# Kernel optimization log

Measured on AMD Instinct MI355X. Metric: run time of the kernel, lower is better.

Reference implementation:

```python
import jax, jax.numpy as jnp
import numpy as np
import math

# dims matching init_kwargs
B, N, CS, CZ = 1, 512, 384, 128
H, C, PQ, PV = 8, 128, 8, 8
INF, EPS = 1e5, 1e-8

# ---- quaternion / motor helpers (PGA motor encoded as [qw,qx,qy,qz,tx,ty,tz,0]) ----

def quat_conj(q):
    return q * jnp.array([1.0, -1.0, -1.0, -1.0], q.dtype)

def quat_mul(a, b):
    aw, ax, ay, az = jnp.split(a, 4, -1)
    bw, bx, by, bz = jnp.split(b, 4, -1)
    return jnp.concatenate([
        aw*bw - ax*bx - ay*by - az*bz,
        aw*bx + ax*bw + ay*bz - az*by,
        aw*by - ax*bz + ay*bw + az*bx,
        aw*bz + ax*by - ay*bx + az*bw], -1)

def quat_rotate(q, v):
    qv = q[..., 1:]
    uv = jnp.cross(qv, v)
    uuv = jnp.cross(qv, uv)
    return v + 2.0 * (q[..., :1] * uv + uuv)

def point_trafo(p, q, t):
    # p [...,K,3]; rigid transform by frame motor, homogeneous 4-vector out
    pp = quat_rotate(q, p) + t
    return jnp.concatenate([pp, jnp.ones_like(pp[..., :1])], -1)

def mv_transform(mv, q, t):
    # versor sandwich on a 16-dim multivector: three rotatable 3-vector blocks,
    # the point block (7:10, weight at 10) also translates; slots 0 and 10:16 invariant
    s0 = mv[..., 0:1]
    v1 = quat_rotate(q, mv[..., 1:4])
    v2 = quat_rotate(q, mv[..., 4:7])
    w = mv[..., 10:11]
    p = quat_rotate(q, mv[..., 7:10]) + w * t
    return jnp.concatenate([s0, v1, v2, p, mv[..., 10:16]], -1)

def mv_transform_inv(mv, q, t):
    qc = quat_conj(q)
    s0 = mv[..., 0:1]
    v1 = quat_rotate(qc, mv[..., 1:4])
    v2 = quat_rotate(qc, mv[..., 4:7])
    w = mv[..., 10:11]
    p = quat_rotate(qc, mv[..., 7:10] - w * t)
    return jnp.concatenate([s0, v1, v2, p, mv[..., 10:16]], -1)


def _forward(s, g, z, T, mask, W_q, b_q, W_kv, b_kv, W_qp, b_qp, W_kp, b_kp,
             W_vg, b_vg, W_mg, W_b, b_b, W_dz, b_dz, head_weights,
             softmax_weights, W_out, b_out, W_geo):
    T8 = T[..., :8]                                      # extract_motor
    qn = T8[..., :4]
    qn = qn / jnp.sqrt(jnp.sum(qn**2, -1, keepdims=True) + EPS)
    tr = T8[..., 4:7]

    q = (s @ W_q + b_q).reshape(B, N, H, C)
    kv = (s @ W_kv + b_kv).reshape(B, N, H, 2 * C)
    k, v = kv[..., :C], kv[..., C:]

    def make_pts(W, bb):
        # split into 3 chunks + stack(dim=-1) == reshape(...,3,HP).swapaxes
        p = (s @ W + bb).reshape(B, N, 3, H * PQ).swapaxes(-1, -2)  # [B,N,HP,3]
        p4 = point_trafo(p, qn[:, :, None, :], tr[:, :, None, :])
        return p4.reshape(B, N, H, PQ, 4)

    q_pts = make_pts(W_qp, b_qp)
    k_pts = make_pts(W_kp, b_kp)

    v_g = (s @ W_vg + b_vg).reshape(B, N, PV, 16)
    v_g = jnp.einsum('oi,bnic->bnoc', W_mg,
                     jnp.concatenate([v_g, g], -2)).reshape(B, N, H, PV, 16)

    bias = jnp.einsum('bijz,zh->bhij', z, W_b) + b_b[None, :, None, None]
    a = jnp.einsum('bihc,bjhc->bhij', q, k) * math.sqrt(1.0 / (3 * C))
    a = a + math.sqrt(1.0 / 3.0) * bias

    disp = q_pts[:, :, None, :, :, :3] - k_pts[:, None, :, :, :, :3]  # [B,N,N,H,P,3]
    pt = jnp.sum(disp**2, -1)                                         # [B,N,N,H,P]
    hw = jax.nn.softplus(head_weights) * math.sqrt(1.0 / (3 * (PQ * 9.0 / 2)))
    pt = -0.5 * jnp.sum(pt * hw[None, None, None, :, None], -1)       # [B,N,N,H]

    sq_mask = INF * (mask[:, :, None] * mask[:, None, :] - 1.0)
    a = a + pt.transpose(0, 3, 1, 2) + sq_mask[:, None]
    a = jax.nn.softmax(softmax_weights[None, :, None, None] * a, axis=-1)

    o = jnp.einsum('bhij,bjhc->bihc', a, v)                           # [B,N,H,C]

    qb, tb = qn[:, :, None, None, :], tr[:, :, None, None, :]
    vg_glob = mv_transform(v_g, qb, tb)
    o_g = jnp.einsum('bhij,bjhpc->bihpc', a, vg_glob)
    o_g = mv_transform_inv(o_g, qb, tb)                               # [B,N,H,PV,16]
    n1 = jnp.sqrt(jnp.sum(o_g[..., :10]**2, -1) + EPS)
    n2 = jnp.sqrt(jnp.sum(o_g[..., 10:]**2, -1) + EPS)
    o_g_norm = jnp.stack([n1, n2], -1)                                # [B,N,H,PV,2]

    # local relative frame features (8 per head)
    q_rel = quat_mul(quat_conj(qn)[:, :, None, :], qn[:, None, :, :])
    t_rel = quat_rotate(quat_conj(qn)[:, :, None, :], tr[:, None, :, :] - tr[:, :, None, :])
    rel = jnp.concatenate([q_rel, t_rel, jnp.zeros_like(t_rel[..., :1])], -1)  # [B,N,N,8]
    o_rel = jnp.einsum('bhij,bijc->bihc', a, rel)

    o_pair = jnp.einsum('bhij,bijc->bihc', a, z @ W_dz + b_dz)        # [B,N,H,CZ//4]

    feats = jnp.concatenate([o_pair, o, o_rel,
                             o_g.reshape(B, N, H, PV * 16),
                             o_g_norm.reshape(B, N, H, PV * 2)], -1).reshape(B, N, -1)
    s_out = feats @ W_out + b_out                                     # [B,N,CS]
    g_out = jnp.einsum('oi,bnic->bnoc', W_geo, o_g.reshape(B, N, H * PV, 16))
    return s_out, g_out


def setup_inputs() -> dict:
    key = jax.random.key(0)
    ks = jax.random.split(key, 32)
    def rn(i, shape, sc=1.0):
        return sc * jax.random.normal(ks[i], shape, jnp.float32)
    s = rn(0, (B, N, CS))
    g = rn(1, (B, N, PV, 16))
    z = rn(2, (B, N, N, CZ))
    Traw = rn(3, (B, N, 16))
    qn = Traw[..., :4]
    qn = qn / jnp.sqrt(jnp.sum(qn**2, -1, keepdims=True) + 1e-8)
    T = Traw.at[..., :4].set(qn).at[..., 4:7].multiply(3.0).at[..., 7:].set(0.0)
    mask = jnp.ones((B, N), jnp.float32)
    w = 0.02
    CAT = H * (CZ // 4 + C + 8 + PV * 18)   # 2496
    return dict(
        s=s, g=g, z=z, T=T, mask=mask,
        W_q=rn(4, (CS, H * C), w), b_q=jnp.zeros((H * C,), jnp.float32),
        W_kv=rn(5, (CS, 2 * H * C), w), b_kv=jnp.zeros((2 * H * C,), jnp.float32),
        W_qp=rn(6, (CS, H * PQ * 3), w), b_qp=jnp.zeros((H * PQ * 3,), jnp.float32),
        W_kp=rn(7, (CS, H * PQ * 3), w), b_kp=jnp.zeros((H * PQ * 3,), jnp.float32),
        W_vg=rn(8, (CS, PV * 16), w), b_vg=jnp.zeros((PV * 16,), jnp.float32),
        W_mg=rn(9, (H * PV, 2 * PV), 0.1),
        W_b=rn(10, (CZ, H), w), b_b=jnp.zeros((H,), jnp.float32),
        W_dz=rn(11, (CZ, CZ // 4), w), b_dz=jnp.zeros((CZ // 4,), jnp.float32),
        head_weights=-2.0 + 0.3 * rn(12, (H,)),
        softmax_weights=jnp.ones((H,), jnp.float32) + 0.1 * rn(13, (H,)),
        W_out=rn(14, (CAT, CS), w), b_out=jnp.zeros((CS,), jnp.float32),
        W_geo=rn(15, (PV, H * PV), 0.1))


def reference(s, g, z, T, mask, W_q, b_q, W_kv, b_kv, W_qp, b_qp, W_kp, b_kp,
              W_vg, b_vg, W_mg, W_b, b_b, W_dz, b_dz, head_weights,
              softmax_weights, W_out, b_out, W_geo):
    return _forward(s, g, z, T, mask, W_q, b_q, W_kv, b_kv, W_qp, b_qp, W_kp,
                    b_kp, W_vg, b_vg, W_mg, W_b, b_b, W_dz, b_dz, head_weights,
                    softmax_weights, W_out, b_out, W_geo)
```

## Files before the change

kernel.cpp:

```cpp
#include <hip/hip_runtime.h>
#include <math.h>

#define NN 512
#define CSD 384
#define CZD 128
#define HD 8
#define CD 128
#define EPSV 1e-8f
#define INFV 100000.0f

#define OFF_QN    ((size_t)0)
#define OFF_TR    ((size_t)2048)
#define OFF_ROWT  ((size_t)4096)
#define OFF_COLT  ((size_t)8192)
#define OFF_SB    ((size_t)12288)
#define OFF_QBUF  ((size_t)45056)
#define OFF_KV    ((size_t)569344)
#define OFF_QPR   ((size_t)1617920)
#define OFF_KPR   ((size_t)1716224)
#define OFF_VGR   ((size_t)1814528)
#define OFF_ZB    ((size_t)1880064)
#define OFF_A     ((size_t)3977216)
#define OFF_U     ((size_t)6074368)
#define OFF_V     ((size_t)6729728)
#define OFF_VP    ((size_t)7385088)
#define OFF_OB0   ((size_t)8433664)
#define OFF_OB1   ((size_t)8957952)
#define OFF_OG0   ((size_t)9482240)
#define OFF_OG1   ((size_t)10006528)
#define OFF_FEATS ((size_t)10530816)
#define OFF_PS    ((size_t)11808768)

typedef __attribute__((ext_vector_type(4))) float f32x4;
typedef __attribute__((ext_vector_type(8))) short bf16x8;
typedef __attribute__((ext_vector_type(4))) short s16x4;

__device__ __forceinline__ void qrot(const float q[4], const float* v, float* out) {
    float qw = q[0], qx = q[1], qy = q[2], qz = q[3];
    float ux = qy*v[2] - qz*v[1];
    float uy = qz*v[0] - qx*v[2];
    float uz = qx*v[1] - qy*v[0];
    float uux = qy*uz - qz*uy;
    float uuy = qz*ux - qx*uz;
    float uuz = qx*uy - qy*ux;
    out[0] = v[0] + 2.0f*(qw*ux + uux);
    out[1] = v[1] + 2.0f*(qw*uy + uuy);
    out[2] = v[2] + 2.0f*(qw*uz + uuz);
}

__device__ __forceinline__ void cvt2(float x, unsigned short& h, unsigned short& lo) {
    unsigned u = __float_as_uint(x);
    unsigned r = (u + 0x7FFFu + ((u >> 16) & 1u)) >> 16;
    h = (unsigned short)r;
    float hf = __uint_as_float(r << 16);
    float lf = x - hf;
    unsigned u2 = __float_as_uint(lf);
    unsigned r2 = (u2 + 0x7FFFu + ((u2 >> 16) & 1u)) >> 16;
    lo = (unsigned short)r2;
}

__device__ __forceinline__ void stA(short* H, short* L, int row, int k4, float4 v) {
    unsigned short h0,l0,h1,l1,h2,l2,h3,l3;
    cvt2(v.x,h0,l0); cvt2(v.y,h1,l1); cvt2(v.z,h2,l2); cvt2(v.w,h3,l3);
    s16x4 vh = {(short)h0,(short)h1,(short)h2,(short)h3};
    s16x4 vl = {(short)l0,(short)l1,(short)l2,(short)l3};
    *(s16x4*)(H + row*40 + k4) = vh;
    *(s16x4*)(L + row*40 + k4) = vl;
}
__device__ __forceinline__ void stBT(short* H, short* L, int k, int n4, float4 v) {
    unsigned short h, lo;
    cvt2(v.x,h,lo); H[(n4+0)*40+k]=(short)h; L[(n4+0)*40+k]=(short)lo;
    cvt2(v.y,h,lo); H[(n4+1)*40+k]=(short)h; L[(n4+1)*40+k]=(short)lo;
    cvt2(v.z,h,lo); H[(n4+2)*40+k]=(short)h; L[(n4+2)*40+k]=(short)lo;
    cvt2(v.w,h,lo); H[(n4+3)*40+k]=(short)h; L[(n4+3)*40+k]=(short)lo;
}

template<int BT>
__device__ __forceinline__ void mfma_tiles(const float* __restrict__ A, int lda,
                                           const float* __restrict__ B, int ldb,
                                           int m0, int n0, int k0, int nk,
                                           f32x4* acc,
                                           short* Ah, short* Al, short* Bh, short* Bl) {
    int t = threadIdx.x;
    int w = t >> 6, l = t & 63, g = l >> 4, li = l & 15;
    int ar = t >> 3, ak = (t & 7) << 2;
    const float* Ap0 = A + (size_t)(m0 + ar)*lda + ak;
    const float* Ap1 = A + (size_t)(m0 + ar + 32)*lda + ak;
    const float* Bp0; const float* Bp1;
    int bk = t >> 4, bn = (t & 15) << 2;
    if (BT) {
        Bp0 = B + (size_t)(n0 + ar)*ldb + ak;
        Bp1 = B + (size_t)(n0 + ar + 32)*ldb + ak;
    } else {
        Bp0 = B + (size_t)bk*ldb + n0 + bn;
        Bp1 = B + (size_t)(bk + 16)*ldb + n0 + bn;
    }
    float4 a0 = *(const float4*)(Ap0 + k0);
    float4 a1 = *(const float4*)(Ap1 + k0);
    float4 b0, b1;
    if (BT) { b0 = *(const float4*)(Bp0 + k0); b1 = *(const float4*)(Bp1 + k0); }
    else    { b0 = *(const float4*)(Bp0 + (size_t)k0*ldb); b1 = *(const float4*)(Bp1 + (size_t)k0*ldb); }
    for (int kc = 0; kc < nk; kc++) {
        stA(Ah, Al, ar, ak, a0);
        stA(Ah, Al, ar+32, ak, a1);
        if (BT) { stA(Bh, Bl, ar, ak, b0); stA(Bh, Bl, ar+32, ak, b1); }
        else    { stBT(Bh, Bl, bk, bn, b0); stBT(Bh, Bl, bk+16, bn, b1); }
        __syncthreads();
        if (kc + 1 < nk) {
            int kb = k0 + (kc+1)*32;
            a0 = *(const float4*)(Ap0 + kb);
            a1 = *(const float4*)(Ap1 + kb);
            if (BT) { b0 = *(const float4*)(Bp0 + kb); b1 = *(const float4*)(Bp1 + kb); }
            else { b0 = *(const float4*)(Bp0 + (size_t)kb*ldb); b1 = *(const float4*)(Bp1 + (size_t)kb*ldb); }
        }
        int arow = (w*16 + li)*40 + g*8;
        bf16x8 avh = *(bf16x8*)(Ah + arow);
        bf16x8 avl = *(bf16x8*)(Al + arow);
        #pragma unroll
        for (int c = 0; c < 4; c++) {
            int brow = (c*16 + li)*40 + g*8;
            bf16x8 bvh = *(bf16x8*)(Bh + brow);
            bf16x8 bvl = *(bf16x8*)(Bl + brow);
            acc[c] = __builtin_amdgcn_mfma_f32_16x16x32_bf16(avh, bvh, acc[c], 0, 0, 0);
            acc[c] = __builtin_amdgcn_mfma_f32_16x16x32_bf16(avh, bvl, acc[c], 0, 0, 0);
            acc[c] = __builtin_amdgcn_mfma_f32_16x16x32_bf16(avl, bvh, acc[c], 0, 0, 0);
        }
        __syncthreads();
    }
}

__device__ __forceinline__ void gemm_tiles(const float* __restrict__ A, int lda,
                                           const float* __restrict__ B, int ldb,
                                           int m0, int n0, int k0, int nk,
                                           float acc[4][4], float* AsT, float* Bs) {
    int t = threadIdx.x;
    int tx = t & 15, ty = t >> 4;
    int arow = t >> 3, ak4 = (t & 7) << 2;
    int brow = t >> 4, bc4 = (t & 15) << 2;
    const float* Ap0 = A + (size_t)(m0 + arow)*lda + ak4;
    const float* Ap1 = A + (size_t)(m0 + arow + 32)*lda + ak4;
    const float* Bp0 = B + (size_t)brow*ldb + n0 + bc4;
    const float* Bp1 = B + (size_t)(brow + 16)*ldb + n0 + bc4;
    float4 a0 = *(const float4*)(Ap0 + k0);
    float4 a1 = *(const float4*)(Ap1 + k0);
    float4 b0 = *(const float4*)(Bp0 + (size_t)k0*ldb);
    float4 b1 = *(const float4*)(Bp1 + (size_t)k0*ldb);
    for (int kc = 0; kc < nk; kc++) {
        AsT[(ak4+0)*68 + arow] = a0.x;
        AsT[(ak4+1)*68 + arow] = a0.y;
        AsT[(ak4+2)*68 + arow] = a0.z;
        AsT[(ak4+3)*68 + arow] = a0.w;
        AsT[(ak4+0)*68 + arow+32] = a1.x;
        AsT[(ak4+1)*68 + arow+32] = a1.y;
        AsT[(ak4+2)*68 + arow+32] = a1.z;
        AsT[(ak4+3)*68 + arow+32] = a1.w;
        *(float4*)(Bs + brow*64 + bc4) = b0;
        *(float4*)(Bs + (brow+16)*64 + bc4) = b1;
        __syncthreads();
        if (kc + 1 < nk) {
            int kb = k0 + (kc+1)*32;
            a0 = *(const float4*)(Ap0 + kb);
            a1 = *(const float4*)(Ap1 + kb);
            b0 = *(const float4*)(Bp0 + (size_t)kb*ldb);
            b1 = *(const float4*)(Bp1 + (size_t)kb*ldb);
        }
        #pragma unroll
        for (int kk = 0; kk < 32; kk++) {
            float4 av = *(const float4*)(AsT + kk*68 + ty*4);
            float4 bv = *(const float4*)(Bs + kk*64 + tx*4);
            acc[0][0] += av.x*bv.x; acc[0][1] += av.x*bv.y; acc[0][2] += av.x*bv.z; acc[0][3] += av.x*bv.w;
            acc[1][0] += av.y*bv.x; acc[1][1] += av.y*bv.y; acc[1][2] += av.y*bv.z; acc[1][3] += av.y*bv.w;
            acc[2][0] += av.z*bv.x; acc[2][1] += av.z*bv.y; acc[2][2] += av.z*bv.z; acc[2][3] += av.z*bv.w;
            acc[3][0] += av.w*bv.x; acc[3][1] += av.w*bv.y; acc[3][2] += av.w*bv.z; acc[3][3] += av.w*bv.w;
        }
        __syncthreads();
    }
}


__global__ __launch_bounds__(256) void k_proj_all(const float* __restrict__ s,
    const float* __restrict__ W_q,  const float* __restrict__ b_q,  float* __restrict__ qbuf,
    const float* __restrict__ W_kv, const float* __restrict__ b_kv, float* __restrict__ kvb,
    const float* __restrict__ W_qp, const float* __restrict__ b_qp, float* __restrict__ qpr,
    const float* __restrict__ W_kp, const float* __restrict__ b_kp, float* __restrict__ kpr,
    const float* __restrict__ W_vg, const float* __restrict__ b_vg, float* __restrict__ vgr) {
    __shared__ float AsT[32*68];
    __shared__ float Bs[32*64];
    int ny = blockIdx.y;
    const float* W; const float* bias; float* C; int N; int n0;
    if (ny < 16)      { W=W_q;  bias=b_q;  C=qbuf; N=1024; n0=ny*64; }
    else if (ny < 48) { W=W_kv; bias=b_kv; C=kvb;  N=2048; n0=(ny-16)*64; }
    else if (ny < 51) { W=W_qp; bias=b_qp; C=qpr;  N=192;  n0=(ny-48)*64; }
    else if (ny < 54) { W=W_kp; bias=b_kp; C=kpr;  N=192;  n0=(ny-51)*64; }
    else              { W=W_vg; bias=b_vg; C=vgr;  N=128;  n0=(ny-54)*64; }
    int m0 = blockIdx.x*64;
    float acc[4][4] = {};
    gemm_tiles(s, CSD, W, N, m0, n0, 0, 12, acc, AsT, Bs);
    int tx = threadIdx.x & 15, ty = threadIdx.x >> 4;
    float4 bb = *(const float4*)(bias + n0 + tx*4);
    #pragma unroll
    for (int rr = 0; rr < 4; rr++) {
        float4 o = make_float4(acc[rr][0]+bb.x, acc[rr][1]+bb.y, acc[rr][2]+bb.z, acc[rr][3]+bb.w);
        *(float4*)(C + (size_t)(m0+ty*4+rr)*N + n0 + tx*4) = o;
    }
}

__global__ __launch_bounds__(256) void k_geo(
    const float* __restrict__ T,
    const float* __restrict__ qpr, const float* __restrict__ kpr,
    const float* __restrict__ vgr, const float* __restrict__ g,
    const float* __restrict__ W_mg,
    const float* __restrict__ qbuf, const float* __restrict__ kvb,
    const float* __restrict__ hwraw, const float* __restrict__ b_b,
    float* __restrict__ qn, float* __restrict__ tr,
    float* __restrict__ U, float* __restrict__ V,
    float* __restrict__ rowt, float* __restrict__ colt,
    float* __restrict__ Vp)
{
    __shared__ float s_q[4];
    __shared__ float s_t[3];
    __shared__ float s_qpts[192], s_kpts[192];
    __shared__ float s_Qsq[8], s_Ksq[8];
    int n = blockIdx.x, t = threadIdx.x;
    if (t == 0) {
        float q0=T[n*16+0], q1=T[n*16+1], q2=T[n*16+2], q3=T[n*16+3];
        float inv = 1.0f/sqrtf(q0*q0+q1*q1+q2*q2+q3*q3 + EPSV);
        float a0=q0*inv, a1=q1*inv, a2=q2*inv, a3=q3*inv;
        s_q[0]=a0; s_q[1]=a1; s_q[2]=a2; s_q[3]=a3;
        float u0=T[n*16+4], u1=T[n*16+5], u2=T[n*16+6];
        s_t[0]=u0; s_t[1]=u1; s_t[2]=u2;
        qn[n*4+0]=a0; qn[n*4+1]=a1; qn[n*4+2]=a2; qn[n*4+3]=a3;
        tr[n*3+0]=u0; tr[n*3+1]=u1; tr[n*3+2]=u2;
    }
    __syncthreads();
    float q[4]={s_q[0],s_q[1],s_q[2],s_q[3]};
    float t0=s_t[0], t1=s_t[1], t2=s_t[2];
    if (t < 128) {
        int m = t & 63;
        const float* raw = (t < 64) ? qpr : kpr;
        float p[3] = {raw[n*192 + m], raw[n*192 + 64 + m], raw[n*192 + 128 + m]};
        float r[3]; qrot(q,p,r);
        r[0]+=t0; r[1]+=t1; r[2]+=t2;
        float* dp = (t<64) ? s_qpts : s_kpts;
        dp[m*3+0]=r[0]; dp[m*3+1]=r[1]; dp[m*3+2]=r[2];
        float ss = r[0]*r[0]+r[1]*r[1]+r[2]*r[2];
        ss += __shfl_down(ss,4,8);
        ss += __shfl_down(ss,2,8);
        ss += __shfl_down(ss,1,8);
        if ((m&7)==0) ((t<64)?s_Qsq:s_Ksq)[m>>3] = ss;
    } else if (t < 192) {
        int o = t - 128;
        float in[16];
        #pragma unroll
        for (int c=0;c<16;c++){
            float acc=0.0f;
            #pragma unroll
            for (int i=0;i<8;i++)  acc += W_mg[o*16+i]*vgr[n*128+i*16+c];
            #pragma unroll
            for (int i=8;i<16;i++) acc += W_mg[o*16+i]*g[n*128+(i-8)*16+c];
            in[c]=acc;
        }
        float out[16];
        out[0]=in[0];
        qrot(q,in+1,out+1);
        qrot(q,in+4,out+4);
        float w=in[10];
        qrot(q,in+7,out+7);
        out[7]+=w*t0; out[8]+=w*t1; out[9]+=w*t2;
        #pragma unroll
        for (int c=10;c<16;c++) out[c]=in[c];
        int h=o>>3, pp=o&7;
        float* vp = Vp + ((size_t)(h*512+n))*256 + 128 + pp*16;
        #pragma unroll
        for (int c=0;c<16;c++) vp[c]=out[c];
    }
    #pragma unroll
    for (int l=0;l<4;l++){
        int f = t + l*256; int h = f>>7, c = f&127;
        Vp[((size_t)(h*512+n))*256 + c] = kvb[(size_t)n*2048 + h*256 + 128 + c];
    }
    __syncthreads();
    #pragma unroll
    for (int h = 0; h < 8; h++) {
        float hwv = log1pf(expf(hwraw[h])) * 0.09622504486493763f;
        if (t < 160) {
            float u, v;
            if (t < 128) {
                u = 0.05103103630798287f * qbuf[(size_t)n*1024 + h*128 + t];
                v = kvb[(size_t)n*2048 + h*256 + t];
            } else if (t < 152) {
                int d = t - 128;
                u = hwv * s_qpts[h*24 + d];
                v = s_kpts[h*24 + d];
            } else { u = 0.0f; v = 0.0f; }
            U[((size_t)h*512 + n)*160 + t] = u;
            V[((size_t)h*512 + n)*160 + t] = v;
        }
        if (t == 160) rowt[h*512+n] = -0.5f*hwv*s_Qsq[h] + 0.5773502691896258f*b_b[h] - INFV;
        if (t == 161) colt[h*512+n] = -0.5f*hwv*s_Ksq[h];
    }
}

__global__ __launch_bounds__(128) void k_zb(const float* __restrict__ z,
        const float* __restrict__ W_b, float* __restrict__ zb) {
    __shared__ float zt[64*132];
    __shared__ float part[8*64];
    int i = blockIdx.x, j0 = blockIdx.y*64;
    int t = threadIdx.x;
    #pragma unroll
    for (int l = 0; l < 16; l++) {
        int f = t + l*128;
        int row = f >> 5, c4 = (f & 31) << 2;
        float4 v = *(const float4*)(z + ((size_t)(i*NN) + j0 + row)*CZD + c4);
        *(float4*)(zt + row*132 + c4) = v;
    }
    __syncthreads();
    int w = t >> 6, j = t & 63;
    int cbase = w*64;
    float acc[8] = {};
    #pragma unroll
    for (int c16 = 0; c16 < 16; c16++) {
        float4 v = *(const float4*)(zt + j*132 + cbase + c16*4);
        int c = cbase + c16*4;
        #pragma unroll
        for (int h = 0; h < 8; h++)
            acc[h] += v.x*W_b[(c+0)*8+h] + v.y*W_b[(c+1)*8+h]
                    + v.z*W_b[(c+2)*8+h] + v.w*W_b[(c+3)*8+h];
    }
    if (w == 1) {
        #pragma unroll
        for (int h = 0; h < 8; h++) part[h*64 + j] = acc[h];
    }
    __syncthreads();
    if (w == 0) {
        #pragma unroll
        for (int h = 0; h < 8; h++)
            zb[((size_t)h*512 + i)*512 + j0 + j] = acc[h] + part[h*64 + j];
    }
}

__global__ __launch_bounds__(256) void k_scorefill(const float* __restrict__ U, const float* __restrict__ V,
        const float* __restrict__ rowt, const float* __restrict__ colt,
        const float* __restrict__ zb, const float* __restrict__ mask,
        const float* __restrict__ sw, float* __restrict__ Am) {
    __shared__ short Ah[64*40], Al[64*40], Bh[64*40], Bl[64*40];
    int h = blockIdx.z;
    int m0 = blockIdx.x*64, n0 = blockIdx.y*64;
    f32x4 acc[4] = {};
    mfma_tiles<1>(U + (size_t)h*512*160, 160, V + (size_t)h*512*160, 160,
                  m0, n0, 0, 5, acc, Ah, Al, Bh, Bl);
    int t = threadIdx.x, w = t >> 6, l = t & 63, g = l >> 4, li = l & 15;
    float swh = sw[h];
    #pragma unroll
    for (int c = 0; c < 4; c++) {
        int j = n0 + c*16 + li;
        float ct = colt[h*512 + j];
        float mj = mask[j];
        #pragma unroll
        for (int r = 0; r < 4; r++) {
            int i = m0 + w*16 + g*4 + r;
            float rt = rowt[h*512 + i];
            float mi = mask[i]*INFV;
            float zv = zb[((size_t)h*512 + i)*512 + j];
            Am[((size_t)h*512 + i)*512 + j] =
                (acc[c][r] + rt + ct + 0.5773502691896258f*zv + mi*mj)*swh;
        }
    }
}

__global__ __launch_bounds__(256) void k_softmax(float* __restrict__ Am,
        const float* __restrict__ qn, const float* __restrict__ tr, float* __restrict__ S) {
    __shared__ float red[8];
    __shared__ float sred[4][8];
    int row = blockIdx.x;
    float* p = Am + (size_t)row*512;
    int t = threadIdx.x;
    float x0 = p[t], x1 = p[t+256];
    float m = fmaxf(x0, x1);
    #pragma unroll
    for (int o = 32; o > 0; o >>= 1) m = fmaxf(m, __shfl_xor(m, o));
    int wv = t >> 6, ln = t & 63;
    if (ln == 0) red[wv] = m;
    __syncthreads();
    m = fmaxf(fmaxf(red[0], red[1]), fmaxf(red[2], red[3]));
    float e0 = expf(x0 - m), e1 = expf(x1 - m);
    float sm = e0 + e1;
    #pragma unroll
    for (int o = 32; o > 0; o >>= 1) sm += __shfl_xor(sm, o);
    __syncthreads();
    if (ln == 0) red[4 + wv] = sm;
    __syncthreads();
    float inv = 1.0f / (red[4]+red[5]+red[6]+red[7]);
    float a0 = e0*inv, a1 = e1*inv;
    p[t] = a0;
    p[t+256] = a1;
    float4 q0 = *(const float4*)(qn + t*4);
    float4 q1 = *(const float4*)(qn + (t+256)*4);
    float acc[8];
    acc[0] = a0*q0.x + a1*q1.x;
    acc[1] = a0*q0.y + a1*q1.y;
    acc[2] = a0*q0.z + a1*q1.z;
    acc[3] = a0*q0.w + a1*q1.w;
    acc[4] = a0*tr[t*3+0] + a1*tr[(t+256)*3+0];
    acc[5] = a0*tr[t*3+1] + a1*tr[(t+256)*3+1];
    acc[6] = a0*tr[t*3+2] + a1*tr[(t+256)*3+2];
    acc[7] = a0 + a1;
    #pragma unroll
    for (int c = 0; c < 8; c++) {
        #pragma unroll
        for (int o = 32; o > 0; o >>= 1) acc[c] += __shfl_xor(acc[c], o);
    }
    if (ln == 0) {
        #pragma unroll
        for (int c = 0; c < 8; c++) sred[wv][c] = acc[c];
    }
    __syncthreads();
    if (t < 8) {
        int h = row >> 9, i = row & 511;
        S[i*64 + h*8 + t] = sred[0][t]+sred[1][t]+sred[2][t]+sred[3][t];
    }
}

__global__ __launch_bounds__(256) void k_apply(const float* __restrict__ Am,
        const float* __restrict__ Vp, float* __restrict__ ob0, float* __restrict__ ob1,
        float* __restrict__ og0, float* __restrict__ og1) {
    __shared__ short Ah[64*40], Al[64*40], Bh[64*40], Bl[64*40];
    int m0 = blockIdx.x*64;
    int n0 = blockIdx.y*64;
    int h = blockIdx.z & 7, js = blockIdx.z >> 3;
    f32x4 acc[4] = {};
    mfma_tiles<0>(Am + (size_t)h*512*512, 512, Vp + (size_t)h*512*256, 256,
                  m0, n0, js*256, 8, acc, Ah, Al, Bh, Bl);
    int t = threadIdx.x, w = t >> 6, l = t & 63, g = l >> 4, li = l & 15;
    float* obuf = js ? ob1 : ob0;
    float* og   = js ? og1 : og0;
    #pragma unroll
    for (int c = 0; c < 4; c++) {
        int col = n0 + c*16 + li;
        float* base = (col < 128) ? (obuf + h*128 + col) : (og + h*128 + col - 128);
        #pragma unroll
        for (int r = 0; r < 4; r++) {
            int i = m0 + w*16 + g*4 + r;
            base[(size_t)i*1024] = acc[c][r];
        }
    }
}

__global__ __launch_bounds__(256) void k_azfin(
    const float* __restrict__ Am, const float* __restrict__ z,
    const float* __restrict__ ob0, const float* __restrict__ ob1,
    const float* __restrict__ og0, const float* __restrict__ og1,
    const float* __restrict__ W_dz, const float* __restrict__ b_dz,
    const float* __restrict__ S, const float* __restrict__ qn, const float* __restrict__ tr,
    const float* __restrict__ W_geo,
    float* __restrict__ feats, float* __restrict__ outg)
{
    __shared__ float aT[512*8];
    __shared__ float part[3*1024];
    __shared__ float s_az[1024];
    __shared__ float s_og[1024];
    int i = blockIdx.x, t = threadIdx.x;
    #pragma unroll
    for (int l = 0; l < 16; l++) {
        int f = t + l*256;
        int h = f >> 9, j = f & 511;
        aT[j*8 + h] = Am[((size_t)h*512 + i)*512 + j];
    }
    __syncthreads();
    int c2 = t & 63, quarter = t >> 6;
    int jb = quarter*128;
    float acc[8][2] = {};
    for (int j = jb; j < jb+128; j++) {
        float2 zv = *(const float2*)(z + ((size_t)(i*NN) + j)*CZD + c2*2);
        float4 a0 = *(const float4*)(aT + j*8);
        float4 a1 = *(const float4*)(aT + j*8 + 4);
        acc[0][0] += a0.x*zv.x; acc[0][1] += a0.x*zv.y;
        acc[1][0] += a0.y*zv.x; acc[1][1] += a0.y*zv.y;
        acc[2][0] += a0.z*zv.x; acc[2][1] += a0.z*zv.y;
        acc[3][0] += a0.w*zv.x; acc[3][1] += a0.w*zv.y;
        acc[4][0] += a1.x*zv.x; acc[4][1] += a1.x*zv.y;
        acc[5][0] += a1.y*zv.x; acc[5][1] += a1.y*zv.y;
        acc[6][0] += a1.z*zv.x; acc[6][1] += a1.z*zv.y;
        acc[7][0] += a1.w*zv.x; acc[7][1] += a1.w*zv.y;
    }
    if (quarter > 0) {
        #pragma unroll
        for (int h = 0; h < 8; h++) {
            part[(quarter-1)*1024 + h*128 + c2*2 + 0] = acc[h][0];
            part[(quarter-1)*1024 + h*128 + c2*2 + 1] = acc[h][1];
        }
    }
    __syncthreads();
    if (quarter == 0) {
        #pragma unroll
        for (int h = 0; h < 8; h++) {
            #pragma unroll
            for (int d = 0; d < 2; d++) {
                s_az[h*128 + c2*2 + d] = acc[h][d] + part[h*128 + c2*2 + d]
                          + part[1024 + h*128 + c2*2 + d] + part[2048 + h*128 + c2*2 + d];
            }
        }
    }
    __syncthreads();
    float* f = feats + (size_t)i*2496;
    #pragma unroll
    for (int l = 0; l < 4; l++) {
        int ff = t + l*256; int h = ff>>7, c = ff&127;
        f[h*312 + 32 + c] = ob0[(size_t)i*1024 + h*128 + c] + ob1[(size_t)i*1024 + h*128 + c];
    }
    {
        int h = t >> 5, cdz = t & 31;
        float a2 = b_dz[cdz];
        #pragma unroll 4
        for (int zc = 0; zc < 128; zc++) a2 += s_az[h*128 + zc]*W_dz[zc*32 + cdz];
        f[h*312 + cdz] = a2;
    }
    float qc0=qn[i*4], qc1=-qn[i*4+1], qc2=-qn[i*4+2], qc3=-qn[i*4+3];
    float t0=tr[i*3], t1=tr[i*3+1], t2=tr[i*3+2];
    if (t < 64) {
        int h = t >> 3, p = t & 7;
        const float* a0 = og0 + (size_t)i*1024 + h*128 + p*16;
        const float* a1 = og1 + (size_t)i*1024 + h*128 + p*16;
        float in[16];
        #pragma unroll
        for (int c=0;c<16;c++) in[c]=a0[c]+a1[c];
        float qc[4]={qc0,qc1,qc2,qc3};
        float out[16];
        out[0]=in[0];
        qrot(qc,in+1,out+1);
        qrot(qc,in+4,out+4);
        float w=in[10];
        float tmp[3]={in[7]-w*t0, in[8]-w*t1, in[9]-w*t2};
        qrot(qc,tmp,out+7);
        #pragma unroll
        for (int c2x=10;c2x<16;c2x++) out[c2x]=in[c2x];
        float n1=EPSV, n2=EPSV;
        #pragma unroll
        for (int c2x=0;c2x<10;c2x++) n1 += out[c2x]*out[c2x];
        #pragma unroll
        for (int c2x=10;c2x<16;c2x++) n2 += out[c2x]*out[c2x];
        n1=sqrtf(n1); n2=sqrtf(n2);
        #pragma unroll
        for (int c2x=0;c2x<16;c2x++){ f[h*312+168+p*16+c2x]=out[c2x]; s_og[t*16+c2x]=out[c2x]; }
        f[h*312+296+p*2]=n1; f[h*312+296+p*2+1]=n2;
    } else if (t < 72) {
        int h = t - 64;
        const float* Sr = S + i*64 + h*8;
        float b0=Sr[0], b1=Sr[1], b2=Sr[2], b3=Sr[3];
        f[h*312+160] = qc0*b0 - qc1*b1 - qc2*b2 - qc3*b3;
        f[h*312+161] = qc0*b1 + qc1*b0 + qc2*b3 - qc3*b2;
        f[h*312+162] = qc0*b2 - qc1*b3 + qc2*b0 + qc3*b1;
        f[h*312+163] = qc0*b3 + qc1*b2 - qc2*b1 + qc3*b0;
        float A = Sr[7];
        float v[3]={Sr[4]-A*t0, Sr[5]-A*t1, Sr[6]-A*t2};
        float qc[4]={qc0,qc1,qc2,qc3};
        float r[3]; qrot(qc,v,r);
        f[h*312+164]=r[0]; f[h*312+165]=r[1]; f[h*312+166]=r[2]; f[h*312+167]=0.0f;
    }
    __syncthreads();
    if (t < 128) {
        int o = (t>>4) & 7, c = t & 15;
        float a3 = 0.0f;
        #pragma unroll 4
        for (int i2=0;i2<64;i2++) a3 += W_geo[o*64+i2]*s_og[i2*16+c];
        outg[(size_t)i*128 + o*16 + c] = a3;
    }
}

__global__ __launch_bounds__(256) void k_sout(const float* __restrict__ feats,
        const float* __restrict__ W_out, float* __restrict__ Ps) {
    __shared__ float AsT[32*68];
    __shared__ float Bs[32*64];
    int m0 = blockIdx.x*64, n0 = blockIdx.y*64, kz = blockIdx.z;
    float acc[4][4] = {};
    gemm_tiles(feats, 2496, W_out, CSD, m0, n0, kz*416, 13, acc, AsT, Bs);
    int tx = threadIdx.x & 15, ty = threadIdx.x >> 4;
    float* slab = Ps + (size_t)kz*512*384;
    #pragma unroll
    for (int rr = 0; rr < 4; rr++) {
        *(float4*)(slab + (size_t)(m0+ty*4+rr)*CSD + n0 + tx*4) =
            make_float4(acc[rr][0], acc[rr][1], acc[rr][2], acc[rr][3]);
    }
}

__global__ __launch_bounds__(256) void k_sout_red(const float* __restrict__ Ps,
        const float* __restrict__ b_out, float* __restrict__ out) {
    int idx = (blockIdx.x*256 + threadIdx.x)*4;
    float4 s = *(const float4*)(b_out + (idx % 384));
    #pragma unroll
    for (int kz = 0; kz < 6; kz++) {
        float4 p = *(const float4*)(Ps + (size_t)kz*196608 + idx);
        s.x += p.x; s.y += p.y; s.z += p.z; s.w += p.w;
    }
    *(float4*)(out + idx) = s;
}


extern "C" void kernel_launch(void* const* d_in, const int* in_sizes, int n_in,
                              void* d_out, int out_size, void* d_ws, size_t ws_size,
                              hipStream_t stream) {
    const float* s     = (const float*)d_in[0];
    const float* g     = (const float*)d_in[1];
    const float* z     = (const float*)d_in[2];
    const float* T     = (const float*)d_in[3];
    const float* mask  = (const float*)d_in[4];
    const float* W_q   = (const float*)d_in[5];
    const float* b_q   = (const float*)d_in[6];
    const float* W_kv  = (const float*)d_in[7];
    const float* b_kv  = (const float*)d_in[8];
    const float* W_qp  = (const float*)d_in[9];
    const float* b_qp  = (const float*)d_in[10];
    const float* W_kp  = (const float*)d_in[11];
    const float* b_kp  = (const float*)d_in[12];
    const float* W_vg  = (const float*)d_in[13];
    const float* b_vg  = (const float*)d_in[14];
    const float* W_mg  = (const float*)d_in[15];
    const float* W_b   = (const float*)d_in[16];
    const float* b_b   = (const float*)d_in[17];
    const float* W_dz  = (const float*)d_in[18];
    const float* b_dz  = (const float*)d_in[19];
    const float* hw    = (const float*)d_in[20];
    const float* sw    = (const float*)d_in[21];
    const float* W_out = (const float*)d_in[22];
    const float* b_out = (const float*)d_in[23];
    const float* W_geo = (const float*)d_in[24];

    float* ws   = (float*)d_ws;
    float* out  = (float*)d_out;

    float* qn   = ws + OFF_QN;
    float* tr   = ws + OFF_TR;
    float* rowt = ws + OFF_ROWT;
    float* colt = ws + OFF_COLT;
    float* Sbuf = ws + OFF_SB;
    float* qbuf = ws + OFF_QBUF;
    float* kvb  = ws + OFF_KV;
    float* qpr  = ws + OFF_QPR;
    float* kpr  = ws + OFF_KPR;
    float* vgr  = ws + OFF_VGR;
    float* zb   = ws + OFF_ZB;
    float* Am   = ws + OFF_A;
    float* U    = ws + OFF_U;
    float* V    = ws + OFF_V;
    float* Vp   = ws + OFF_VP;
    float* ob0  = ws + OFF_OB0;
    float* ob1  = ws + OFF_OB1;
    float* og0  = ws + OFF_OG0;
    float* og1  = ws + OFF_OG1;
    float* feats= ws + OFF_FEATS;
    float* Ps   = ws + OFF_PS;

    k_proj_all<<<dim3(8,56),256,0,stream>>>(s, W_q,b_q,qbuf, W_kv,b_kv,kvb,
                                            W_qp,b_qp,qpr, W_kp,b_kp,kpr, W_vg,b_vg,vgr);
    k_geo<<<NN,256,0,stream>>>(T,qpr,kpr,vgr,g,W_mg,qbuf,kvb,hw,b_b,
                               qn,tr,U,V,rowt,colt,Vp);
    k_zb<<<dim3(NN,8),128,0,stream>>>(z,W_b,zb);
    k_scorefill<<<dim3(8,8,8),256,0,stream>>>(U,V,rowt,colt,zb,mask,sw,Am);
    k_softmax<<<4096,256,0,stream>>>(Am,qn,tr,Sbuf);
    k_apply<<<dim3(8,4,16),256,0,stream>>>(Am,Vp,ob0,ob1,og0,og1);
    k_azfin<<<NN,256,0,stream>>>(Am,z,ob0,ob1,og0,og1,W_dz,b_dz,Sbuf,qn,tr,W_geo,
                                 feats, out + (size_t)NN*CSD);
    k_sout<<<dim3(8,6,6),256,0,stream>>>(feats,W_out,Ps);
    k_sout_red<<<192,256,0,stream>>>(Ps,b_out,out);
}
```

Before: 402.1 us.

## Pre-split operands into bf16 hi/lo arrays and run all GEMMs on MFMA

Adds a k_split kernel that converts s, the projection weights (transposed) and W_out into separate bf16 high/low arrays. Producer kernels (k_geo, k_softmax, k_azfin) now write U, V, Vp, attention probabilities and feats directly in split-bf16 form. The projection and output GEMMs change from an FP32 SIMT shared-memory tiling to 3-pass bf16 MFMA reading fragments straight from global memory. The aim is to stop re-converting operands inside every GEMM tile and to use the matrix cores for the projection and output GEMMs. In exchange there is an extra launch, more workspace, and scattered 16-bit stores in the producer kernels.

```diff
diff --git a/kernel.cpp b/kernel.cpp
--- a/kernel.cpp
+++ b/kernel.cpp
@@ -21,19 +21,32 @@
 #define OFF_VGR   ((size_t)1814528)
 #define OFF_ZB    ((size_t)1880064)
 #define OFF_A     ((size_t)3977216)
-#define OFF_U     ((size_t)6074368)
-#define OFF_V     ((size_t)6729728)
-#define OFF_VP    ((size_t)7385088)
-#define OFF_OB0   ((size_t)8433664)
-#define OFF_OB1   ((size_t)8957952)
-#define OFF_OG0   ((size_t)9482240)
-#define OFF_OG1   ((size_t)10006528)
-#define OFF_FEATS ((size_t)10530816)
-#define OFF_PS    ((size_t)11808768)
+#define OFF_AMH   ((size_t)6074368)
+#define OFF_AML   ((size_t)7122944)
+#define OFF_UH    ((size_t)8171520)
+#define OFF_UL    ((size_t)8499200)
+#define OFF_VH    ((size_t)8826880)
+#define OFF_VL    ((size_t)9154560)
+#define OFF_VPH   ((size_t)9482240)
+#define OFF_VPL   ((size_t)10006528)
+#define OFF_OB0   ((size_t)10530816)
+#define OFF_OB1   ((size_t)11055104)
+#define OFF_OG0   ((size_t)11579392)
+#define OFF_OG1   ((size_t)12103680)
+#define OFF_FH    ((size_t)12627968)
+#define OFF_FL    ((size_t)13266944)
+#define OFF_PS    ((size_t)13905920)
+#define OFF_SH    ((size_t)15085568)
+#define OFF_SL    ((size_t)15183872)
+#define OFF_WTH   ((size_t)15282176)
+#define OFF_WTL   ((size_t)15970304)
+#define OFF_WOH   ((size_t)16658432)
+#define OFF_WOL   ((size_t)17137664)
 
 typedef __attribute__((ext_vector_type(4))) float f32x4;
 typedef __attribute__((ext_vector_type(8))) short bf16x8;
 typedef __attribute__((ext_vector_type(4))) short s16x4;
+typedef unsigned short u16;
 
 __device__ __forceinline__ void qrot(const float q[4], const float* v, float* out) {
     float qw = q[0], qx = q[1], qy = q[2], qz = q[3];
@@ -48,160 +61,148 @@
     out[2] = v[2] + 2.0f*(qw*uz + uuz);
 }
 
-__device__ __forceinline__ void cvt2(float x, unsigned short& h, unsigned short& lo) {
+__device__ __forceinline__ void cvt2(float x, u16& h, u16& lo) {
     unsigned u = __float_as_uint(x);
     unsigned r = (u + 0x7FFFu + ((u >> 16) & 1u)) >> 16;
-    h = (unsigned short)r;
+    h = (u16)r;
     float hf = __uint_as_float(r << 16);
     float lf = x - hf;
     unsigned u2 = __float_as_uint(lf);
     unsigned r2 = (u2 + 0x7FFFu + ((u2 >> 16) & 1u)) >> 16;
-    lo = (unsigned short)r2;
-}
-
-__device__ __forceinline__ void stA(short* H, short* L, int row, int k4, float4 v) {
-    unsigned short h0,l0,h1,l1,h2,l2,h3,l3;
-    cvt2(v.x,h0,l0); cvt2(v.y,h1,l1); cvt2(v.z,h2,l2); cvt2(v.w,h3,l3);
-    s16x4 vh = {(short)h0,(short)h1,(short)h2,(short)h3};
-    s16x4 vl = {(short)l0,(short)l1,(short)l2,(short)l3};
-    *(s16x4*)(H + row*40 + k4) = vh;
-    *(s16x4*)(L + row*40 + k4) = vl;
-}
-__device__ __forceinline__ void stBT(short* H, short* L, int k, int n4, float4 v) {
-    unsigned short h, lo;
-    cvt2(v.x,h,lo); H[(n4+0)*40+k]=(short)h; L[(n4+0)*40+k]=(short)lo;
-    cvt2(v.y,h,lo); H[(n4+1)*40+k]=(short)h; L[(n4+1)*40+k]=(short)lo;
-    cvt2(v.z,h,lo); H[(n4+2)*40+k]=(short)h; L[(n4+2)*40+k]=(short)lo;
-    cvt2(v.w,h,lo); H[(n4+3)*40+k]=(short)h; L[(n4+3)*40+k]=(short)lo;
-}
-
-template<int BT>
-__device__ __forceinline__ void mfma_tiles(const float* __restrict__ A, int lda,
-                                           const float* __restrict__ B, int ldb,
-                                           int m0, int n0, int k0, int nk,
-                                           f32x4* acc,
-                                           short* Ah, short* Al, short* Bh, short* Bl) {
-    int t = threadIdx.x;
-    int w = t >> 6, l = t & 63, g = l >> 4, li = l & 15;
-    int ar = t >> 3, ak = (t & 7) << 2;
-    const float* Ap0 = A + (size_t)(m0 + ar)*lda + ak;
-    const float* Ap1 = A + (size_t)(m0 + ar + 32)*lda + ak;
-    const float* Bp0; const float* Bp1;
-    int bk = t >> 4, bn = (t & 15) << 2;
-    if (BT) {
-        Bp0 = B + (size_t)(n0 + ar)*ldb + ak;
-        Bp1 = B + (size_t)(n0 + ar + 32)*ldb + ak;
+    lo = (u16)r2;
+}
+__device__ __forceinline__ float bf2f(u16 h) { return __uint_as_float((unsigned)h << 16); }
+
+#define MFMA3(acc, avh, avl, bvh, bvl) \
+    acc = __builtin_amdgcn_mfma_f32_16x16x32_bf16(avh, bvh, acc, 0, 0, 0); \
+    acc = __builtin_amdgcn_mfma_f32_16x16x32_bf16(avh, bvl, acc, 0, 0, 0); \
+    acc = __builtin_amdgcn_mfma_f32_16x16x32_bf16(avl, bvh, acc, 0, 0, 0);
+
+
+__global__ __launch_bounds__(256) void k_split(
+    const float* __restrict__ s, const float* __restrict__ W_q, const float* __restrict__ W_kv,
+    const float* __restrict__ W_qp, const float* __restrict__ W_kp, const float* __restrict__ W_vg,
+    const float* __restrict__ W_out,
+    u16* __restrict__ sh_, u16* __restrict__ sl_,
+    u16* __restrict__ WTh, u16* __restrict__ WTl,
+    u16* __restrict__ WOh, u16* __restrict__ WOl)
+{
+    __shared__ float tile[64*68];
+    int task = blockIdx.z, bx = blockIdx.x, by = blockIdx.y, t = threadIdx.x;
+    if (task == 0) {
+        if (by >= 6) return;
+        const float* W; int ldn, sn0;
+        if (bx < 16)      { W = W_q;  ldn = 1024; sn0 = bx*64; }
+        else if (bx < 48) { W = W_kv; ldn = 2048; sn0 = (bx-16)*64; }
+        else if (bx < 51) { W = W_qp; ldn = 192;  sn0 = (bx-48)*64; }
+        else if (bx < 54) { W = W_kp; ldn = 192;  sn0 = (bx-51)*64; }
+        else              { W = W_vg; ldn = 128;  sn0 = (bx-54)*64; }
+        int k0 = by*64;
+        #pragma unroll
+        for (int lp = 0; lp < 4; lp++) {
+            int kk = (t>>4) + lp*16, nn = (t&15)*4;
+            float4 v = *(const float4*)(W + (size_t)(k0+kk)*ldn + sn0 + nn);
+            tile[kk*68+nn]=v.x; tile[kk*68+nn+1]=v.y; tile[kk*68+nn+2]=v.z; tile[kk*68+nn+3]=v.w;
+        }
+        __syncthreads();
+        #pragma unroll
+        for (int lp = 0; lp < 4; lp++) {
+            int nn = (t>>4) + lp*16, kk4 = (t&15)*4;
+            s16x4 vh, vl;
+            #pragma unroll
+            for (int e = 0; e < 4; e++) {
+                u16 h, lo; cvt2(tile[(kk4+e)*68 + nn], h, lo);
+                vh[e] = (short)h; vl[e] = (short)lo;
+            }
+            size_t o = (size_t)(bx*64 + nn)*384 + k0 + kk4;
+            *(s16x4*)(WTh + o) = vh;
+            *(s16x4*)(WTl + o) = vl;
+        }
+    } else if (task == 1) {
+        if (bx >= 6 || by >= 39) return;
+        int n0 = bx*64, k0 = by*64;
+        #pragma unroll
+        for (int lp = 0; lp < 4; lp++) {
+            int kk = (t>>4) + lp*16, nn = (t&15)*4;
+            float4 v = *(const float4*)(W_out + (size_t)(k0+kk)*384 + n0 + nn);
+            tile[kk*68+nn]=v.x; tile[kk*68+nn+1]=v.y; tile[kk*68+nn+2]=v.z; tile[kk*68+nn+3]=v.w;
+        }
+        __syncthreads();
+        #pragma unroll
+        for (int lp = 0; lp < 4; lp++) {
+            int nn = (t>>4) + lp*16, kk4 = (t&15)*4;
+            s16x4 vh, vl;
+            #pragma unroll
+            for (int e = 0; e < 4; e++) {
+                u16 h, lo; cvt2(tile[(kk4+e)*68 + nn], h, lo);
+                vh[e] = (short)h; vl[e] = (short)lo;
+            }
+            size_t o = (size_t)(n0 + nn)*2496 + k0 + kk4;
+            *(s16x4*)(WOh + o) = vh;
+            *(s16x4*)(WOl + o) = vl;
+        }
     } else {
-        Bp0 = B + (size_t)bk*ldb + n0 + bn;
-        Bp1 = B + (size_t)(bk + 16)*ldb + n0 + bn;
-    }
-    float4 a0 = *(const float4*)(Ap0 + k0);
-    float4 a1 = *(const float4*)(Ap1 + k0);
-    float4 b0, b1;
-    if (BT) { b0 = *(const float4*)(Bp0 + k0); b1 = *(const float4*)(Bp1 + k0); }
-    else    { b0 = *(const float4*)(Bp0 + (size_t)k0*ldb); b1 = *(const float4*)(Bp1 + (size_t)k0*ldb); }
-    for (int kc = 0; kc < nk; kc++) {
-        stA(Ah, Al, ar, ak, a0);
-        stA(Ah, Al, ar+32, ak, a1);
-        if (BT) { stA(Bh, Bl, ar, ak, b0); stA(Bh, Bl, ar+32, ak, b1); }
-        else    { stBT(Bh, Bl, bk, bn, b0); stBT(Bh, Bl, bk+16, bn, b1); }
-        __syncthreads();
-        if (kc + 1 < nk) {
-            int kb = k0 + (kc+1)*32;
-            a0 = *(const float4*)(Ap0 + kb);
-            a1 = *(const float4*)(Ap1 + kb);
-            if (BT) { b0 = *(const float4*)(Bp0 + kb); b1 = *(const float4*)(Bp1 + kb); }
-            else { b0 = *(const float4*)(Bp0 + (size_t)kb*ldb); b1 = *(const float4*)(Bp1 + (size_t)kb*ldb); }
-        }
-        int arow = (w*16 + li)*40 + g*8;
-        bf16x8 avh = *(bf16x8*)(Ah + arow);
-        bf16x8 avl = *(bf16x8*)(Al + arow);
+        if (bx >= 8 || by >= 6) return;
+        int m0 = bx*64, k0 = by*64;
+        #pragma unroll
+        for (int lp = 0; lp < 4; lp++) {
+            int row = (t>>4) + lp*16, c4 = (t&15)*4;
+            float4 v = *(const float4*)(s + (size_t)(m0+row)*384 + k0 + c4);
+            s16x4 vh, vl;
+            u16 h, lo;
+            cvt2(v.x,h,lo); vh[0]=(short)h; vl[0]=(short)lo;
+            cvt2(v.y,h,lo); vh[1]=(short)h; vl[1]=(short)lo;
+            cvt2(v.z,h,lo); vh[2]=(short)h; vl[2]=(short)lo;
+            cvt2(v.w,h,lo); vh[3]=(short)h; vl[3]=(short)lo;
+            size_t o = (size_t)(m0+row)*384 + k0 + c4;
+            *(s16x4*)(sh_ + o) = vh;
+            *(s16x4*)(sl_ + o) = vl;
+        }
+    }
+}
+
+__global__ __launch_bounds__(256) void k_proj_all(
+    const u16* __restrict__ sh_, const u16* __restrict__ sl_,
+    const u16* __restrict__ WTh, const u16* __restrict__ WTl,
+    const float* __restrict__ b_q,  float* __restrict__ qbuf,
+    const float* __restrict__ b_kv, float* __restrict__ kvb,
+    const float* __restrict__ b_qp, float* __restrict__ qpr,
+    const float* __restrict__ b_kp, float* __restrict__ kpr,
+    const float* __restrict__ b_vg, float* __restrict__ vgr)
+{
+    int ny = blockIdx.y;
+    const float* bias; float* C; int N, n0, base;
+    if (ny < 16)      { bias=b_q;  C=qbuf; N=1024; n0=ny*64;      base=0; }
+    else if (ny < 48) { bias=b_kv; C=kvb;  N=2048; n0=(ny-16)*64; base=1024; }
+    else if (ny < 51) { bias=b_qp; C=qpr;  N=192;  n0=(ny-48)*64; base=3072; }
+    else if (ny < 54) { bias=b_kp; C=kpr;  N=192;  n0=(ny-51)*64; base=3264; }
+    else              { bias=b_vg; C=vgr;  N=128;  n0=(ny-54)*64; base=3456; }
+    int m0 = blockIdx.x*64;
+    int t = threadIdx.x, w = t>>6, l = t&63, g = l>>4, li = l&15;
+    const u16* Ah = sh_ + (size_t)(m0 + w*16 + li)*384 + g*8;
+    const u16* Al = sl_ + (size_t)(m0 + w*16 + li)*384 + g*8;
+    const u16* Bh0 = WTh + (size_t)(base + n0 + li)*384 + g*8;
+    const u16* Bl0 = WTl + (size_t)(base + n0 + li)*384 + g*8;
+    f32x4 acc[4] = {};
+    for (int ks = 0; ks < 12; ks++) {
+        bf16x8 avh = *(const bf16x8*)(Ah + ks*32);
+        bf16x8 avl = *(const bf16x8*)(Al + ks*32);
         #pragma unroll
         for (int c = 0; c < 4; c++) {
-            int brow = (c*16 + li)*40 + g*8;
-            bf16x8 bvh = *(bf16x8*)(Bh + brow);
-            bf16x8 bvl = *(bf16x8*)(Bl + brow);
-            acc[c] = __builtin_amdgcn_mfma_f32_16x16x32_bf16(avh, bvh, acc[c], 0, 0, 0);
-            acc[c] = __builtin_amdgcn_mfma_f32_16x16x32_bf16(avh, bvl, acc[c], 0, 0, 0);
-            acc[c] = __builtin_amdgcn_mfma_f32_16x16x32_bf16(avl, bvh, acc[c], 0, 0, 0);
-        }
-        __syncthreads();
-    }
-}
-
-__device__ __forceinline__ void gemm_tiles(const float* __restrict__ A, int lda,
-                                           const float* __restrict__ B, int ldb,
-                                           int m0, int n0, int k0, int nk,
-                                           float acc[4][4], float* AsT, float* Bs) {
-    int t = threadIdx.x;
-    int tx = t & 15, ty = t >> 4;
-    int arow = t >> 3, ak4 = (t & 7) << 2;
-    int brow = t >> 4, bc4 = (t & 15) << 2;
-    const float* Ap0 = A + (size_t)(m0 + arow)*lda + ak4;
-    const float* Ap1 = A + (size_t)(m0 + arow + 32)*lda + ak4;
-    const float* Bp0 = B + (size_t)brow*ldb + n0 + bc4;
-    const float* Bp1 = B + (size_t)(brow + 16)*ldb + n0 + bc4;
-    float4 a0 = *(const float4*)(Ap0 + k0);
-    float4 a1 = *(const float4*)(Ap1 + k0);
-    float4 b0 = *(const float4*)(Bp0 + (size_t)k0*ldb);
-    float4 b1 = *(const float4*)(Bp1 + (size_t)k0*ldb);
-    for (int kc = 0; kc < nk; kc++) {
-        AsT[(ak4+0)*68 + arow] = a0.x;
-        AsT[(ak4+1)*68 + arow] = a0.y;
-        AsT[(ak4+2)*68 + arow] = a0.z;
-        AsT[(ak4+3)*68 + arow] = a0.w;
-        AsT[(ak4+0)*68 + arow+32] = a1.x;
-        AsT[(ak4+1)*68 + arow+32] = a1.y;
-        AsT[(ak4+2)*68 + arow+32] = a1.z;
-        AsT[(ak4+3)*68 + arow+32] = a1.w;
-        *(float4*)(Bs + brow*64 + bc4) = b0;
-        *(float4*)(Bs + (brow+16)*64 + bc4) = b1;
-        __syncthreads();
-        if (kc + 1 < nk) {
-            int kb = k0 + (kc+1)*32;
-            a0 = *(const float4*)(Ap0 + kb);
-            a1 = *(const float4*)(Ap1 + kb);
-            b0 = *(const float4*)(Bp0 + (size_t)kb*ldb);
-            b1 = *(const float4*)(Bp1 + (size_t)kb*ldb);
-        }
-        #pragma unroll
-        for (int kk = 0; kk < 32; kk++) {
-            float4 av = *(const float4*)(AsT + kk*68 + ty*4);
-            float4 bv = *(const float4*)(Bs + kk*64 + tx*4);
-            acc[0][0] += av.x*bv.x; acc[0][1] += av.x*bv.y; acc[0][2] += av.x*bv.z; acc[0][3] += av.x*bv.w;
-            acc[1][0] += av.y*bv.x; acc[1][1] += av.y*bv.y; acc[1][2] += av.y*bv.z; acc[1][3] += av.y*bv.w;
-            acc[2][0] += av.z*bv.x; acc[2][1] += av.z*bv.y; acc[2][2] += av.z*bv.z; acc[2][3] += av.z*bv.w;
-            acc[3][0] += av.w*bv.x; acc[3][1] += av.w*bv.y; acc[3][2] += av.w*bv.z; acc[3][3] += av.w*bv.w;
-        }
-        __syncthreads();
-    }
-}
-
-
-__global__ __launch_bounds__(256) void k_proj_all(const float* __restrict__ s,
-    const float* __restrict__ W_q,  const float* __restrict__ b_q,  float* __restrict__ qbuf,
-    const float* __restrict__ W_kv, const float* __restrict__ b_kv, float* __restrict__ kvb,
-    const float* __restrict__ W_qp, const float* __restrict__ b_qp, float* __restrict__ qpr,
-    const float* __restrict__ W_kp, const float* __restrict__ b_kp, float* __restrict__ kpr,
-    const float* __restrict__ W_vg, const float* __restrict__ b_vg, float* __restrict__ vgr) {
-    __shared__ float AsT[32*68];
-    __shared__ float Bs[32*64];
-    int ny = blockIdx.y;
-    const float* W; const float* bias; float* C; int N; int n0;
-    if (ny < 16)      { W=W_q;  bias=b_q;  C=qbuf; N=1024; n0=ny*64; }
-    else if (ny < 48) { W=W_kv; bias=b_kv; C=kvb;  N=2048; n0=(ny-16)*64; }
-    else if (ny < 51) { W=W_qp; bias=b_qp; C=qpr;  N=192;  n0=(ny-48)*64; }
-    else if (ny < 54) { W=W_kp; bias=b_kp; C=kpr;  N=192;  n0=(ny-51)*64; }
-    else              { W=W_vg; bias=b_vg; C=vgr;  N=128;  n0=(ny-54)*64; }
-    int m0 = blockIdx.x*64;
-    float acc[4][4] = {};
-    gemm_tiles(s, CSD, W, N, m0, n0, 0, 12, acc, AsT, Bs);
-    int tx = threadIdx.x & 15, ty = threadIdx.x >> 4;
-    float4 bb = *(const float4*)(bias + n0 + tx*4);
-    #pragma unroll
-    for (int rr = 0; rr < 4; rr++) {
-        float4 o = make_float4(acc[rr][0]+bb.x, acc[rr][1]+bb.y, acc[rr][2]+bb.z, acc[rr][3]+bb.w);
-        *(float4*)(C + (size_t)(m0+ty*4+rr)*N + n0 + tx*4) = o;
+            bf16x8 bvh = *(const bf16x8*)(Bh0 + (size_t)c*16*384 + ks*32);
+            bf16x8 bvl = *(const bf16x8*)(Bl0 + (size_t)c*16*384 + ks*32);
+            MFMA3(acc[c], avh, avl, bvh, bvl);
+        }
+    }
+    #pragma unroll
+    for (int c = 0; c < 4; c++) {
+        int col = n0 + c*16 + li;
+        float bb = bias[col];
+        #pragma unroll
+        for (int r = 0; r < 4; r++) {
+            int row = m0 + w*16 + g*4 + r;
+            C[(size_t)row*N + col] = acc[c][r] + bb;
+        }
     }
 }
 
@@ -213,9 +214,10 @@
     const float* __restrict__ qbuf, const float* __restrict__ kvb,
     const float* __restrict__ hwraw, const float* __restrict__ b_b,
     float* __restrict__ qn, float* __restrict__ tr,
-    float* __restrict__ U, float* __restrict__ V,
+    u16* __restrict__ Uh, u16* __restrict__ Ul,
+    u16* __restrict__ Vh, u16* __restrict__ Vl,
     float* __restrict__ rowt, float* __restrict__ colt,
-    float* __restrict__ Vp)
+    u16* __restrict__ Vph, u16* __restrict__ Vpl)
 {
     __shared__ float s_q[4];
     __shared__ float s_t[3];
@@ -270,14 +272,19 @@
         #pragma unroll
         for (int c=10;c<16;c++) out[c]=in[c];
         int h=o>>3, pp=o&7;
-        float* vp = Vp + ((size_t)(h*512+n))*256 + 128 + pp*16;
-        #pragma unroll
-        for (int c=0;c<16;c++) vp[c]=out[c];
+        size_t vb = ((size_t)(h*512+n))*256 + 128 + pp*16;
+        #pragma unroll
+        for (int c=0;c<16;c++) {
+            u16 hh, ll; cvt2(out[c], hh, ll);
+            Vph[vb+c]=hh; Vpl[vb+c]=ll;
+        }
     }
     #pragma unroll
     for (int l=0;l<4;l++){
         int f = t + l*256; int h = f>>7, c = f&127;
-        Vp[((size_t)(h*512+n))*256 + c] = kvb[(size_t)n*2048 + h*256 + 128 + c];
+        u16 hh, ll; cvt2(kvb[(size_t)n*2048 + h*256 + 128 + c], hh, ll);
+        Vph[((size_t)(h*512+n))*256 + c] = hh;
+        Vpl[((size_t)(h*512+n))*256 + c] = ll;
     }
     __syncthreads();
     #pragma unroll
@@ -293,8 +300,10 @@
                 u = hwv * s_qpts[h*24 + d];
                 v = s_kpts[h*24 + d];
             } else { u = 0.0f; v = 0.0f; }
-            U[((size_t)h*512 + n)*160 + t] = u;
-            V[((size_t)h*512 + n)*160 + t] = v;
+            size_t o = ((size_t)h*512 + n)*160 + t;
+            u16 hh, ll;
+            cvt2(u, hh, ll); Uh[o]=hh; Ul[o]=ll;
+            cvt2(v, hh, ll); Vh[o]=hh; Vl[o]=ll;
         }
         if (t == 160) rowt[h*512+n] = -0.5f*hwv*s_Qsq[h] + 0.5773502691896258f*b_b[h] - INFV;
         if (t == 161) colt[h*512+n] = -0.5f*hwv*s_Ksq[h];
@@ -339,17 +348,31 @@
     }
 }
 
-__global__ __launch_bounds__(256) void k_scorefill(const float* __restrict__ U, const float* __restrict__ V,
+__global__ __launch_bounds__(256) void k_scorefill(
+        const u16* __restrict__ Uh, const u16* __restrict__ Ul,
+        const u16* __restrict__ Vh, const u16* __restrict__ Vl,
         const float* __restrict__ rowt, const float* __restrict__ colt,
         const float* __restrict__ zb, const float* __restrict__ mask,
         const float* __restrict__ sw, float* __restrict__ Am) {
-    __shared__ short Ah[64*40], Al[64*40], Bh[64*40], Bl[64*40];
     int h = blockIdx.z;
     int m0 = blockIdx.x*64, n0 = blockIdx.y*64;
+    int t = threadIdx.x, w = t>>6, l = t&63, g = l>>4, li = l&15;
+    const u16* Ah = Uh + ((size_t)h*512 + m0 + w*16 + li)*160 + g*8;
+    const u16* Al = Ul + ((size_t)h*512 + m0 + w*16 + li)*160 + g*8;
+    const u16* Bh0 = Vh + ((size_t)h*512 + n0 + li)*160 + g*8;
+    const u16* Bl0 = Vl + ((size_t)h*512 + n0 + li)*160 + g*8;
     f32x4 acc[4] = {};
-    mfma_tiles<1>(U + (size_t)h*512*160, 160, V + (size_t)h*512*160, 160,
-                  m0, n0, 0, 5, acc, Ah, Al, Bh, Bl);
-    int t = threadIdx.x, w = t >> 6, l = t & 63, g = l >> 4, li = l & 15;
+    #pragma unroll
+    for (int ks = 0; ks < 5; ks++) {
+        bf16x8 avh = *(const bf16x8*)(Ah + ks*32);
+        bf16x8 avl = *(const bf16x8*)(Al + ks*32);
+        #pragma unroll
+        for (int c = 0; c < 4; c++) {
+            bf16x8 bvh = *(const bf16x8*)(Bh0 + (size_t)c*16*160 + ks*32);
+            bf16x8 bvl = *(const bf16x8*)(Bl0 + (size_t)c*16*160 + ks*32);
+            MFMA3(acc[c], avh, avl, bvh, bvl);
+        }
+    }
     float swh = sw[h];
     #pragma unroll
     for (int c = 0; c < 4; c++) {
@@ -368,12 +391,13 @@
     }
 }
 
-__global__ __launch_bounds__(256) void k_softmax(float* __restrict__ Am,
+__global__ __launch_bounds__(256) void k_softmax(const float* __restrict__ Am,
+        u16* __restrict__ Amh, u16* __restrict__ Aml,
         const float* __restrict__ qn, const float* __restrict__ tr, float* __restrict__ S) {
     __shared__ float red[8];
     __shared__ float sred[4][8];
     int row = blockIdx.x;
-    float* p = Am + (size_t)row*512;
+    const float* p = Am + (size_t)row*512;
     int t = threadIdx.x;
     float x0 = p[t], x1 = p[t+256];
     float m = fmaxf(x0, x1);
@@ -392,8 +416,9 @@
     __syncthreads();
     float inv = 1.0f / (red[4]+red[5]+red[6]+red[7]);
     float a0 = e0*inv, a1 = e1*inv;
-    p[t] = a0;
-    p[t+256] = a1;
+    u16 hh, ll;
+    cvt2(a0, hh, ll); Amh[(size_t)row*512 + t] = hh;     Aml[(size_t)row*512 + t] = ll;
+    cvt2(a1, hh, ll); Amh[(size_t)row*512 + t+256] = hh; Aml[(size_t)row*512 + t+256] = ll;
     float4 q0 = *(const float4*)(qn + t*4);
     float4 q1 = *(const float4*)(qn + (t+256)*4);
     float acc[8];
@@ -421,17 +446,60 @@
     }
 }
 
-__global__ __launch_bounds__(256) void k_apply(const float* __restrict__ Am,
-        const float* __restrict__ Vp, float* __restrict__ ob0, float* __restrict__ ob1,
+__global__ __launch_bounds__(256) void k_apply(
+        const u16* __restrict__ Amh, const u16* __restrict__ Aml,
+        const u16* __restrict__ Vph, const u16* __restrict__ Vpl,
+        float* __restrict__ ob0, float* __restrict__ ob1,
         float* __restrict__ og0, float* __restrict__ og1) {
-    __shared__ short Ah[64*40], Al[64*40], Bh[64*40], Bl[64*40];
+    __shared__ u16 sBh[2][64*48];
+    __shared__ u16 sBl[2][64*48];
     int m0 = blockIdx.x*64;
     int n0 = blockIdx.y*64;
     int h = blockIdx.z & 7, js = blockIdx.z >> 3;
+    int t = threadIdx.x, w = t>>6, l = t&63, g = l>>4, li = l&15;
+    int jl = t>>3, c8 = (t&7)*8;
+    int jsw = jl ^ (((c8>>3)&3)<<3);
+    const u16* Ah = Amh + ((size_t)h*512 + m0 + w*16 + li)*512 + js*256 + g*8;
+    const u16* Al = Aml + ((size_t)h*512 + m0 + w*16 + li)*512 + js*256 + g*8;
     f32x4 acc[4] = {};
-    mfma_tiles<0>(Am + (size_t)h*512*512, 512, Vp + (size_t)h*512*256, 256,
-                  m0, n0, js*256, 8, acc, Ah, Al, Bh, Bl);
-    int t = threadIdx.x, w = t >> 6, l = t & 63, g = l >> 4, li = l & 15;
+    {
+        const u16* srcH = Vph + ((size_t)h*512 + js*256 + jl)*256 + n0 + c8;
+        const u16* srcL = Vpl + ((size_t)h*512 + js*256 + jl)*256 + n0 + c8;
+        bf16x8 vh = *(const bf16x8*)srcH;
+        bf16x8 vl = *(const bf16x8*)srcL;
+        #pragma unroll
+        for (int e = 0; e < 8; e++) {
+            sBh[0][(c8+e)*48 + jsw] = (u16)vh[e];
+            sBl[0][(c8+e)*48 + jsw] = (u16)vl[e];
+        }
+    }
+    __syncthreads();
+    for (int kc = 0; kc < 8; kc++) {
+        int cur = kc & 1;
+        if (kc + 1 < 8) {
+            int koff = js*256 + (kc+1)*32;
+            const u16* srcH = Vph + ((size_t)h*512 + koff + jl)*256 + n0 + c8;
+            const u16* srcL = Vpl + ((size_t)h*512 + koff + jl)*256 + n0 + c8;
+            bf16x8 vh = *(const bf16x8*)srcH;
+            bf16x8 vl = *(const bf16x8*)srcL;
+            #pragma unroll
+            for (int e = 0; e < 8; e++) {
+                sBh[cur^1][(c8+e)*48 + jsw] = (u16)vh[e];
+                sBl[cur^1][(c8+e)*48 + jsw] = (u16)vl[e];
+            }
+        }
+        bf16x8 avh = *(const bf16x8*)(Ah + kc*32);
+        bf16x8 avl = *(const bf16x8*)(Al + kc*32);
+        #pragma unroll
+        for (int c = 0; c < 4; c++) {
+            int col = c*16 + li;
+            int gp = g ^ ((col>>3)&3);
+            bf16x8 bvh = *(const bf16x8*)(&sBh[cur][col*48 + gp*8]);
+            bf16x8 bvl = *(const bf16x8*)(&sBl[cur][col*48 + gp*8]);
+            MFMA3(acc[c], avh, avl, bvh, bvl);
+        }
+        __syncthreads();
+    }
     float* obuf = js ? ob1 : ob0;
     float* og   = js ? og1 : og0;
     #pragma unroll
@@ -447,13 +515,13 @@
 }
 
 __global__ __launch_bounds__(256) void k_azfin(
-    const float* __restrict__ Am, const float* __restrict__ z,
+    const u16* __restrict__ Amh, const u16* __restrict__ Aml, const float* __restrict__ z,
     const float* __restrict__ ob0, const float* __restrict__ ob1,
     const float* __restrict__ og0, const float* __restrict__ og1,
     const float* __restrict__ W_dz, const float* __restrict__ b_dz,
     const float* __restrict__ S, const float* __restrict__ qn, const float* __restrict__ tr,
     const float* __restrict__ W_geo,
-    float* __restrict__ feats, float* __restrict__ outg)
+    u16* __restrict__ fh, u16* __restrict__ fl, float* __restrict__ outg)
 {
     __shared__ float aT[512*8];
     __shared__ float part[3*1024];
@@ -464,7 +532,8 @@
     for (int l = 0; l < 16; l++) {
         int f = t + l*256;
         int h = f >> 9, j = f & 511;
-        aT[j*8 + h] = Am[((size_t)h*512 + i)*512 + j];
+        size_t idx = ((size_t)h*512 + i)*512 + j;
+        aT[j*8 + h] = bf2f(Amh[idx]) + bf2f(Aml[idx]);
     }
     __syncthreads();
     int c2 = t & 63, quarter = t >> 6;
@@ -502,18 +571,20 @@
         }
     }
     __syncthreads();
-    float* f = feats + (size_t)i*2496;
+    size_t fb = (size_t)i*2496;
+    u16 hh, ll;
     #pragma unroll
     for (int l = 0; l < 4; l++) {
         int ff = t + l*256; int h = ff>>7, c = ff&127;
-        f[h*312 + 32 + c] = ob0[(size_t)i*1024 + h*128 + c] + ob1[(size_t)i*1024 + h*128 + c];
+        float v = ob0[(size_t)i*1024 + h*128 + c] + ob1[(size_t)i*1024 + h*128 + c];
+        cvt2(v, hh, ll); fh[fb + h*312 + 32 + c] = hh; fl[fb + h*312 + 32 + c] = ll;
     }
     {
         int h = t >> 5, cdz = t & 31;
         float a2 = b_dz[cdz];
         #pragma unroll 4
         for (int zc = 0; zc < 128; zc++) a2 += s_az[h*128 + zc]*W_dz[zc*32 + cdz];
-        f[h*312 + cdz] = a2;
+        cvt2(a2, hh, ll); fh[fb + h*312 + cdz] = hh; fl[fb + h*312 + cdz] = ll;
     }
     float qc0=qn[i*4], qc1=-qn[i*4+1], qc2=-qn[i*4+2], qc3=-qn[i*4+3];
     float t0=tr[i*3], t1=tr[i*3+1], t2=tr[i*3+2];
@@ -541,21 +612,33 @@
         for (int c2x=10;c2x<16;c2x++) n2 += out[c2x]*out[c2x];
         n1=sqrtf(n1); n2=sqrtf(n2);
         #pragma unroll
-        for (int c2x=0;c2x<16;c2x++){ f[h*312+168+p*16+c2x]=out[c2x]; s_og[t*16+c2x]=out[c2x]; }
-        f[h*312+296+p*2]=n1; f[h*312+296+p*2+1]=n2;
+        for (int c2x=0;c2x<16;c2x++){
+            cvt2(out[c2x], hh, ll);
+            fh[fb + h*312+168+p*16+c2x] = hh; fl[fb + h*312+168+p*16+c2x] = ll;
+            s_og[t*16+c2x]=out[c2x];
+        }
+        cvt2(n1, hh, ll); fh[fb + h*312+296+p*2]   = hh; fl[fb + h*312+296+p*2]   = ll;
+        cvt2(n2, hh, ll); fh[fb + h*312+296+p*2+1] = hh; fl[fb + h*312+296+p*2+1] = ll;
     } else if (t < 72) {
         int h = t - 64;
         const float* Sr = S + i*64 + h*8;
         float b0=Sr[0], b1=Sr[1], b2=Sr[2], b3=Sr[3];
-        f[h*312+160] = qc0*b0 - qc1*b1 - qc2*b2 - qc3*b3;
-        f[h*312+161] = qc0*b1 + qc1*b0 + qc2*b3 - qc3*b2;
-        f[h*312+162] = qc0*b2 - qc1*b3 + qc2*b0 + qc3*b1;
-        f[h*312+163] = qc0*b3 + qc1*b2 - qc2*b1 + qc3*b0;
+        float o0 = qc0*b0 - qc1*b1 - qc2*b2 - qc3*b3;
+        float o1 = qc0*b1 + qc1*b0 + qc2*b3 - qc3*b2;
+        float o2 = qc0*b2 - qc1*b3 + qc2*b0 + qc3*b1;
+        float o3 = qc0*b3 + qc1*b2 - qc2*b1 + qc3*b0;
         float A = Sr[7];
         float v[3]={Sr[4]-A*t0, Sr[5]-A*t1, Sr[6]-A*t2};
         float qc[4]={qc0,qc1,qc2,qc3};
         float r[3]; qrot(qc,v,r);
-        f[h*312+164]=r[0]; f[h*312+165]=r[1]; f[h*312+166]=r[2]; f[h*312+167]=0.0f;
+        cvt2(o0,hh,ll);  fh[fb+h*312+160]=hh; fl[fb+h*312+160]=ll;
+        cvt2(o1,hh,ll);  fh[fb+h*312+161]=hh; fl[fb+h*312+161]=ll;
+        cvt2(o2,hh,ll);  fh[fb+h*312+162]=hh; fl[fb+h*312+162]=ll;
+        cvt2(o3,hh,ll);  fh[fb+h*312+163]=hh; fl[fb+h*312+163]=ll;
+        cvt2(r[0],hh,ll);fh[fb+h*312+164]=hh; fl[fb+h*312+164]=ll;
+        cvt2(r[1],hh,ll);fh[fb+h*312+165]=hh; fl[fb+h*312+165]=ll;
+        cvt2(r[2],hh,ll);fh[fb+h*312+166]=hh; fl[fb+h*312+166]=ll;
+        fh[fb+h*312+167]=0; fl[fb+h*312+167]=0;
     }
     __syncthreads();
     if (t < 128) {
@@ -567,19 +650,36 @@
     }
 }
 
-__global__ __launch_bounds__(256) void k_sout(const float* __restrict__ feats,
-        const float* __restrict__ W_out, float* __restrict__ Ps) {
-    __shared__ float AsT[32*68];
-    __shared__ float Bs[32*64];
+__global__ __launch_bounds__(256) void k_sout(
+        const u16* __restrict__ fh, const u16* __restrict__ fl,
+        const u16* __restrict__ WOh, const u16* __restrict__ WOl,
+        float* __restrict__ Ps) {
     int m0 = blockIdx.x*64, n0 = blockIdx.y*64, kz = blockIdx.z;
-    float acc[4][4] = {};
-    gemm_tiles(feats, 2496, W_out, CSD, m0, n0, kz*416, 13, acc, AsT, Bs);
-    int tx = threadIdx.x & 15, ty = threadIdx.x >> 4;
+    int t = threadIdx.x, w = t>>6, l = t&63, g = l>>4, li = l&15;
+    const u16* Ah = fh + (size_t)(m0 + w*16 + li)*2496 + kz*416 + g*8;
+    const u16* Al = fl + (size_t)(m0 + w*16 + li)*2496 + kz*416 + g*8;
+    const u16* Bh0 = WOh + (size_t)(n0 + li)*2496 + kz*416 + g*8;
+    const u16* Bl0 = WOl + (size_t)(n0 + li)*2496 + kz*416 + g*8;
+    f32x4 acc[4] = {};
+    for (int ks = 0; ks < 13; ks++) {
+        bf16x8 avh = *(const bf16x8*)(Ah + ks*32);
+        bf16x8 avl = *(const bf16x8*)(Al + ks*32);
+        #pragma unroll
+        for (int c = 0; c < 4; c++) {
+            bf16x8 bvh = *(const bf16x8*)(Bh0 + (size_t)c*16*2496 + ks*32);
+            bf16x8 bvl = *(const bf16x8*)(Bl0 + (size_t)c*16*2496 + ks*32);
+            MFMA3(acc[c], avh, avl, bvh, bvl);
+        }
+    }
     float* slab = Ps + (size_t)kz*512*384;
     #pragma unroll
-    for (int rr = 0; rr < 4; rr++) {
-        *(float4*)(slab + (size_t)(m0+ty*4+rr)*CSD + n0 + tx*4) =
-            make_float4(acc[rr][0], acc[rr][1], acc[rr][2], acc[rr][3]);
+    for (int c = 0; c < 4; c++) {
+        int col = n0 + c*16 + li;
+        #pragma unroll
+        for (int r = 0; r < 4; r++) {
+            int row = m0 + w*16 + g*4 + r;
+            slab[(size_t)row*CSD + col] = acc[c][r];
+        }
     }
 }
 
@@ -640,26 +740,40 @@
     float* vgr  = ws + OFF_VGR;
     float* zb   = ws + OFF_ZB;
     float* Am   = ws + OFF_A;
-    float* U    = ws + OFF_U;
-    float* V    = ws + OFF_V;
-    float* Vp   = ws + OFF_VP;
+    u16* Amh    = (u16*)(ws + OFF_AMH);
+    u16* Aml    = (u16*)(ws + OFF_AML);
+    u16* Uh     = (u16*)(ws + OFF_UH);
+    u16* Ul     = (u16*)(ws + OFF_UL);
+    u16* Vh     = (u16*)(ws + OFF_VH);
+    u16* Vl     = (u16*)(ws + OFF_VL);
+    u16* Vph    = (u16*)(ws + OFF_VPH);
+    u16* Vpl    = (u16*)(ws + OFF_VPL);
     float* ob0  = ws + OFF_OB0;
     float* ob1  = ws + OFF_OB1;
     float* og0  = ws + OFF_OG0;
     float* og1  = ws + OFF_OG1;
-    float* feats= ws + OFF_FEATS;
+    u16* fh     = (u16*)(ws + OFF_FH);
+    u16* fl     = (u16*)(ws + OFF_FL);
     float* Ps   = ws + OFF_PS;
-
-    k_proj_all<<<dim3(8,56),256,0,stream>>>(s, W_q,b_q,qbuf, W_kv,b_kv,kvb,
-                                            W_qp,b_qp,qpr, W_kp,b_kp,kpr, W_vg,b_vg,vgr);
+    u16* sh_    = (u16*)(ws + OFF_SH);
+    u16* sl_    = (u16*)(ws + OFF_SL);
+    u16* WTh    = (u16*)(ws + OFF_WTH);
+    u16* WTl    = (u16*)(ws + OFF_WTL);
+    u16* WOh    = (u16*)(ws + OFF_WOH);
+    u16* WOl    = (u16*)(ws + OFF_WOL);
+
+    k_split<<<dim3(56,39,3),256,0,stream>>>(s,W_q,W_kv,W_qp,W_kp,W_vg,W_out,
+                                            sh_,sl_,WTh,WTl,WOh,WOl);
+    k_proj_all<<<dim3(8,56),256,0,stream>>>(sh_,sl_,WTh,WTl,
+                                            b_q,qbuf, b_kv,kvb, b_qp,qpr, b_kp,kpr, b_vg,vgr);
     k_geo<<<NN,256,0,stream>>>(T,qpr,kpr,vgr,g,W_mg,qbuf,kvb,hw,b_b,
-                               qn,tr,U,V,rowt,colt,Vp);
+                               qn,tr,Uh,Ul,Vh,Vl,rowt,colt,Vph,Vpl);
     k_zb<<<dim3(NN,8),128,0,stream>>>(z,W_b,zb);
-    k_scorefill<<<dim3(8,8,8),256,0,stream>>>(U,V,rowt,colt,zb,mask,sw,Am);
-    k_softmax<<<4096,256,0,stream>>>(Am,qn,tr,Sbuf);
-    k_apply<<<dim3(8,4,16),256,0,stream>>>(Am,Vp,ob0,ob1,og0,og1);
-    k_azfin<<<NN,256,0,stream>>>(Am,z,ob0,ob1,og0,og1,W_dz,b_dz,Sbuf,qn,tr,W_geo,
-                                 feats, out + (size_t)NN*CSD);
-    k_sout<<<dim3(8,6,6),256,0,stream>>>(feats,W_out,Ps);
+    k_scorefill<<<dim3(8,8,8),256,0,stream>>>(Uh,Ul,Vh,Vl,rowt,colt,zb,mask,sw,Am);
+    k_softmax<<<4096,256,0,stream>>>(Am,Amh,Aml,qn,tr,Sbuf);
+    k_apply<<<dim3(8,4,16),256,0,stream>>>(Amh,Aml,Vph,Vpl,ob0,ob1,og0,og1);
+    k_azfin<<<NN,256,0,stream>>>(Amh,Aml,z,ob0,ob1,og0,og1,W_dz,b_dz,Sbuf,qn,tr,W_geo,
+                                 fh,fl, out + (size_t)NN*CSD);
+    k_sout<<<dim3(8,6,6),256,0,stream>>>(fh,fl,WOh,WOl,Ps);
     k_sout_red<<<192,256,0,stream>>>(Ps,b_out,out);
 }
```

New measurement: 409.6 us. About the same (+1.9%).
